# Kernel optimization log

Hardware: AMD Instinct MI355X
Metric: run time of the kernel (lower is better)

Reference implementation:

```python
import jax, jax.numpy as jnp
import numpy as np
import math

HIDDEN = 1024
NUM_HEADS = 16
HEAD_DIM = 64
NUM_PREV = 4
BATCH = 4
SEQ = 1024
ROPE_BASE = 10000.0


def _rope(x):
    """Apply rotary embedding to x [..., seq, head_dim] (rotate-half form)."""
    d = x.shape[-1]
    s = x.shape[-2]
    inv_freq = 1.0 / (ROPE_BASE ** (jnp.arange(0, d, 2, dtype=jnp.float32) / d))
    ang = jnp.arange(s, dtype=jnp.float32)[:, None] * inv_freq[None, :]  # [s, d/2]
    cos, sin = jnp.cos(ang), jnp.sin(ang)
    x1, x2 = jnp.split(x, 2, axis=-1)
    return jnp.concatenate([x1 * cos - x2 * sin, x1 * sin + x2 * cos], axis=-1)


def setup_inputs() -> dict:
    key = jax.random.key(0)
    ks = jax.random.split(key, 8)
    std = 0.02
    d = {
        "hidden_states": jax.random.normal(ks[0], (BATCH, SEQ, HIDDEN), jnp.float32),
        "prev_hidden_states": jax.random.normal(ks[1], (NUM_PREV, BATCH, SEQ, HIDDEN), jnp.float32),
        "wq": jax.random.normal(ks[2], (HIDDEN, NUM_HEADS * HEAD_DIM), jnp.float32) * std,
        "bq": jnp.zeros((NUM_HEADS * HEAD_DIM,), jnp.float32),
        "wk": jax.random.normal(ks[3], (HIDDEN, NUM_HEADS * HEAD_DIM), jnp.float32) * std,
        "bk": jnp.zeros((NUM_HEADS * HEAD_DIM,), jnp.float32),
        "wv": jax.random.normal(ks[4], (HIDDEN, NUM_HEADS * HEAD_DIM), jnp.float32) * std,
        "bv": jnp.zeros((NUM_HEADS * HEAD_DIM,), jnp.float32),
        "wo": jax.random.normal(ks[5], (NUM_HEADS * HEAD_DIM, HIDDEN), jnp.float32) * std,
        "bo": jnp.zeros((HIDDEN,), jnp.float32),
        "wg": jax.random.normal(ks[6], (HIDDEN, NUM_PREV), jnp.float32) * std,
    }
    return d


def reference(hidden_states, prev_hidden_states, wq, bq, wk, bk, wv, bv, wo, bo, wg):
    B, S, H = hidden_states.shape
    P = prev_hidden_states.shape[0]
    nh, hd = NUM_HEADS, HEAD_DIM

    # Q projection + split heads + RoPE: [b, h, s, d]
    q = (hidden_states @ wq + bq).reshape(B, S, nh, hd).transpose(0, 2, 1, 3)
    q = _rope(q)

    # K/V projections for all prev layers at once: [p, b, h, s, d]
    k = (jnp.einsum('pbsh,he->pbse', prev_hidden_states, wk) + bk)
    k = k.reshape(P, B, S, nh, hd).transpose(0, 1, 3, 2, 4)
    k = _rope(k)
    v = (jnp.einsum('pbsh,he->pbse', prev_hidden_states, wv) + bv)
    v = v.reshape(P, B, S, nh, hd).transpose(0, 1, 3, 2, 4)

    # Attention per prev layer
    scale = 1.0 / math.sqrt(hd)
    attn = jnp.einsum('bhqd,pbhkd->pbhqk', q, k) * scale
    attn = jax.nn.softmax(attn, axis=-1)
    out = jnp.einsum('pbhqk,pbhkd->pbhqd', attn, v)  # [p, b, h, s, d]
    out = out.transpose(0, 1, 3, 2, 4).reshape(P, B, S, H)

    # Learned layer gating (faithful to original broadcast: requires B == P)
    pooled = jnp.mean(hidden_states, axis=1)            # [b, hidden]
    layer_w = jax.nn.softmax(pooled @ wg, axis=-1)      # [b, p]
    combined = jnp.sum(out * layer_w[:, :, None, None], axis=0)  # [b, s, hidden]

    return combined @ wo + bo
```

## Files before the change

kernel.cpp:

```cpp
#include <hip/hip_runtime.h>
#include <hip/hip_bf16.h>

#define B_  4
#define S_  1024
#define H_  1024
#define NH  16
#define HD  64
#define P_  4

typedef __attribute__((ext_vector_type(8))) short bf16x8;
typedef __attribute__((ext_vector_type(4))) float f32x4;

__device__ __forceinline__ float b2f(short s) {
  union { unsigned int u; float f; } v;
  v.u = ((unsigned int)(unsigned short)s) << 16;
  return v.f;
}
__device__ __forceinline__ short f2b(float f) {
  __hip_bfloat16 h = __float2bfloat16(f);
  return *reinterpret_cast<short*>(&h);
}
__device__ __forceinline__ float fast_exp2(float x) {
  float r;
  asm volatile("v_exp_f32 %0, %1" : "=v"(r) : "v"(x));
  return r;
}
__device__ __forceinline__ void gload_lds16(const void* g, void* l) {
  __builtin_amdgcn_global_load_lds(
      (const __attribute__((address_space(1))) unsigned int*)((uintptr_t)g),
      (__attribute__((address_space(3))) unsigned int*)((uintptr_t)l),
      16, 0, 0);
}

__global__ void prep_kernel(const float* __restrict__ hidden, const float* __restrict__ prev,
                            const float* __restrict__ wq, const float* __restrict__ wk,
                            const float* __restrict__ wv, const float* __restrict__ wo,
                            short* __restrict__ hbf, short* __restrict__ pbf,
                            short* __restrict__ wqT, short* __restrict__ wkT,
                            short* __restrict__ wvT, short* __restrict__ woT,
                            float* __restrict__ cost, float* __restrict__ sint,
                            float* __restrict__ pooled) {
  __shared__ short tile[32][33];
  int bid = blockIdx.x, tid = threadIdx.x;
  if (bid < 10240) {
    const float* src; short* dst; int idx;
    if (bid < 2048) { src = hidden; dst = hbf; idx = bid * 256 + tid; }
    else            { src = prev;   dst = pbf; idx = (bid - 2048) * 256 + tid; }
    const float4* s4 = (const float4*)(src + (size_t)idx * 8);
    float4 a = s4[0], b = s4[1];
    bf16x8 pk;
    pk[0] = f2b(a.x); pk[1] = f2b(a.y); pk[2] = f2b(a.z); pk[3] = f2b(a.w);
    pk[4] = f2b(b.x); pk[5] = f2b(b.y); pk[6] = f2b(b.z); pk[7] = f2b(b.w);
    *(bf16x8*)(dst + (size_t)idx * 8) = pk;
  } else if (bid < 14336) {
    int tb = bid - 10240;
    int z = tb >> 10, t = tb & 1023;
    const float* src = (z == 0) ? wq : (z == 1) ? wk : (z == 2) ? wv : wo;
    short*       dst = (z == 0) ? wqT : (z == 1) ? wkT : (z == 2) ? wvT : woT;
    int tx = tid & 31, ty = tid >> 5;
    int c0 = (t & 31) * 32, r0 = (t >> 5) * 32;
#pragma unroll
    for (int i = 0; i < 4; ++i)
      tile[ty + 8 * i][tx] = f2b(src[(r0 + ty + 8 * i) * 1024 + c0 + tx]);
    __syncthreads();
#pragma unroll
    for (int i = 0; i < 4; ++i)
      dst[(c0 + ty + 8 * i) * 1024 + r0 + tx] = tile[tx][ty + 8 * i];
  } else if (bid < 14464) {
    int idx = (bid - 14336) * 256 + tid;
    int s = idx >> 5, i = idx & 31;
    float invf = expf(-(float)i * (logf(10000.0f) / 32.0f));
    float a = (float)s * invf;
    cost[idx] = cosf(a);
    sint[idx] = sinf(a);
  } else {
    int idx = (bid - 14464) * 256 + tid;
    int b = idx >> 10, e = idx & 1023;
    const float* hp = hidden + (size_t)b * S_ * H_ + e;
    float s = 0.f;
    for (int t = 0; t < S_; ++t) s += hp[t * H_];
    pooled[idx] = s * (1.0f / 1024.0f);
  }
}

__global__ void gate_kernel(const float* __restrict__ pooled, const float* __restrict__ wg,
                            float* __restrict__ lw) {
  int w = threadIdx.x >> 6, lane = threadIdx.x & 63;
  float a0 = 0.f, a1 = 0.f, a2 = 0.f, a3 = 0.f;
  for (int e = lane; e < 1024; e += 64) {
    float pv = pooled[w * 1024 + e];
    a0 += pv * wg[e * 4 + 0];
    a1 += pv * wg[e * 4 + 1];
    a2 += pv * wg[e * 4 + 2];
    a3 += pv * wg[e * 4 + 3];
  }
#pragma unroll
  for (int off = 32; off > 0; off >>= 1) {
    a0 += __shfl_xor(a0, off, 64);
    a1 += __shfl_xor(a1, off, 64);
    a2 += __shfl_xor(a2, off, 64);
    a3 += __shfl_xor(a3, off, 64);
  }
  if (lane == 0) {
    float mx = fmaxf(fmaxf(a0, a1), fmaxf(a2, a3));
    float e0 = expf(a0 - mx), e1 = expf(a1 - mx), e2 = expf(a2 - mx), e3 = expf(a3 - mx);
    float inv = 1.0f / (e0 + e1 + e2 + e3);
    lw[w * 4 + 0] = e0 * inv;
    lw[w * 4 + 1] = e1 * inv;
    lw[w * 4 + 2] = e2 * inv;
    lw[w * 4 + 3] = e3 * inv;
  }
}

__device__ __forceinline__ void rope_epilogue(const f32x4 (&acc)[4][4], const float* __restrict__ bias,
                                              short* __restrict__ outp,
                                              const float* __restrict__ cost,
                                              const float* __restrict__ sint,
                                              int m0, int wm, int quad, int c, int hh) {
  float b0 = bias[hh * 64 + c];
  float b1 = bias[hh * 64 + 16 + c];
  float b2_ = bias[hh * 64 + 32 + c];
  float b3 = bias[hh * 64 + 48 + c];
#pragma unroll
  for (int mt = 0; mt < 4; ++mt) {
    int gm = m0 + wm * 64 + mt * 16 + quad * 4;
#pragma unroll
    for (int j = 0; j < 4; ++j) {
      int m = gm + j;
      int s = m & 1023;
      int bbx = m >> 10;
      int orow = ((bbx * NH + hh) * S_ + s) * HD;
      float c0f = cost[s * 32 + c], s0f = sint[s * 32 + c];
      float x1 = acc[mt][0][j] + b0, x2 = acc[mt][2][j] + b2_;
      outp[orow + c]      = f2b(x1 * c0f - x2 * s0f);
      outp[orow + 32 + c] = f2b(x1 * s0f + x2 * c0f);
      float c1f = cost[s * 32 + 16 + c], s1f = sint[s * 32 + 16 + c];
      float y1 = acc[mt][1][j] + b1, y2 = acc[mt][3][j] + b3;
      outp[orow + 16 + c] = f2b(y1 * c1f - y2 * s1f);
      outp[orow + 48 + c] = f2b(y1 * s1f + y2 * c1f);
    }
  }
}

__launch_bounds__(256, 2)
__global__ void qkv_gemm(const short* __restrict__ hbf, const short* __restrict__ pbf,
                         const short* __restrict__ BTq, const short* __restrict__ BTk,
                         const short* __restrict__ BTv,
                         const float* __restrict__ bq, const float* __restrict__ bk,
                         const float* __restrict__ bv,
                         short* __restrict__ outq, short* __restrict__ outk,
                         short* __restrict__ outv,
                         const float* __restrict__ cost, const float* __restrict__ sint) {
  __shared__ __align__(16) short As[128 * 64];
  __shared__ __align__(16) short Bs1[128 * 64];
  __shared__ __align__(16) short Bs2[128 * 64];
  int id = blockIdx.x;
  int xcd = id & 7;
  int local = id >> 3;
  int n0i = local & 7;
  int yl = local >> 3;
  int y = yl * 8 + xcd;
  int tid = threadIdx.x;
  int lane = tid & 63, wvv = tid >> 6;
  int quad = lane >> 4, c = lane & 15;
  int wm = wvv & 1, wn = wvv >> 1;
  bool isQ = y < 32;
  int m0 = (isQ ? y : (y - 32)) * 128;
  int n0 = n0i * 128;
  const short* A  = isQ ? hbf : pbf;
  const short* B1 = isQ ? BTq : BTk;
  f32x4 acc1[4][4] = {}, acc2[4][4] = {};
  const short* Ab = A + (size_t)m0 * 1024;
  const short* Bb1 = B1 + (size_t)n0 * 1024;
  const short* Bb2 = BTv + (size_t)n0 * 1024;
  int sr = tid >> 3, sch = tid & 7;

  for (int kb = 0; kb < 16; ++kb) {
    int k0 = kb * 64;
    __syncthreads();
#pragma unroll
    for (int rd = 0; rd < 4; ++rd) {
      int row = sr + rd * 32;
      int col = ((sch ^ (row & 7)) * 8) + k0;
      gload_lds16(Ab + row * 1024 + col,  As  + rd * 2048 + tid * 8);
      gload_lds16(Bb1 + row * 1024 + col, Bs1 + rd * 2048 + tid * 8);
      if (!isQ) gload_lds16(Bb2 + row * 1024 + col, Bs2 + rd * 2048 + tid * 8);
    }
    __syncthreads();
#pragma unroll
    for (int ko = 0; ko < 2; ++ko) {
      bf16x8 af[4], b1f[4];
#pragma unroll
      for (int mt = 0; mt < 4; ++mt) {
        int row = wm * 64 + mt * 16 + c;
        af[mt] = *(const bf16x8*)&As[row * 64 + (((ko * 4 + quad) ^ (row & 7)) * 8)];
      }
#pragma unroll
      for (int nt = 0; nt < 4; ++nt) {
        int row = wn * 64 + nt * 16 + c;
        b1f[nt] = *(const bf16x8*)&Bs1[row * 64 + (((ko * 4 + quad) ^ (row & 7)) * 8)];
      }
#pragma unroll
      for (int mt = 0; mt < 4; ++mt)
#pragma unroll
        for (int nt = 0; nt < 4; ++nt)
          acc1[mt][nt] = __builtin_amdgcn_mfma_f32_16x16x32_bf16(af[mt], b1f[nt], acc1[mt][nt], 0, 0, 0);
      if (!isQ) {
        bf16x8 b2f_[4];
#pragma unroll
        for (int nt = 0; nt < 4; ++nt) {
          int row = wn * 64 + nt * 16 + c;
          b2f_[nt] = *(const bf16x8*)&Bs2[row * 64 + (((ko * 4 + quad) ^ (row & 7)) * 8)];
        }
#pragma unroll
        for (int mt = 0; mt < 4; ++mt)
#pragma unroll
          for (int nt = 0; nt < 4; ++nt)
            acc2[mt][nt] = __builtin_amdgcn_mfma_f32_16x16x32_bf16(af[mt], b2f_[nt], acc2[mt][nt], 0, 0, 0);
      }
    }
  }

  int colb = n0 + wn * 64;
  int hh = colb >> 6;
  if (isQ) {
    rope_epilogue(acc1, bq, outq, cost, sint, m0, wm, quad, c, hh);
  } else {
    rope_epilogue(acc1, bk, outk, cost, sint, m0, wm, quad, c, hh);
    float bb[4];
#pragma unroll
    for (int nt = 0; nt < 4; ++nt) bb[nt] = bv[hh * 64 + nt * 16 + c];
#pragma unroll
    for (int mt = 0; mt < 4; ++mt) {
      int gm = m0 + wm * 64 + mt * 16 + quad * 4;
      int s4 = gm & 1023, pb = gm >> 10;
#pragma unroll
      for (int nt = 0; nt < 4; ++nt) {
        int d = nt * 16 + c;
        ushort4 pk;
        pk.x = (unsigned short)f2b(acc2[mt][nt][0] + bb[nt]);
        pk.y = (unsigned short)f2b(acc2[mt][nt][1] + bb[nt]);
        pk.z = (unsigned short)f2b(acc2[mt][nt][2] + bb[nt]);
        pk.w = (unsigned short)f2b(acc2[mt][nt][3] + bb[nt]);
        *(ushort4*)&outv[((pb * NH + hh) * HD + d) * S_ + s4] = pk;
      }
    }
  }
}

__launch_bounds__(256, 3)
__global__ void attn_kernel(const short* __restrict__ q, const short* __restrict__ k,
                            const short* __restrict__ vt, short* __restrict__ o) {
  int blk = blockIdx.x;
  int x = blk & 7, qt = (blk >> 3) & 7, g = blk >> 6;
  int pbh = g * 8 + x;
  int b = (pbh >> 4) & 3, h = pbh & 15;
  int tid = threadIdx.x;
  int w = tid >> 6, lane = tid & 63, quad = lane >> 4, c = lane & 15;
  int c7 = c & 7;

  __shared__ __align__(16) short Klds[64 * 64];
  __shared__ __align__(16) short Vlds[64 * 64];
  __shared__ __align__(16) short Plds[4][32 * 64];
  __shared__ float lsumf[4][32];

  const short* qbase = q + ((size_t)(b * NH + h) * S_ + qt * 128 + w * 32 + c) * HD;
  bf16x8 aq[2][2];
#pragma unroll
  for (int mi = 0; mi < 2; ++mi) {
    aq[mi][0] = *(const bf16x8*)(qbase + mi * 16 * HD + quad * 8);
    aq[mi][1] = *(const bf16x8*)(qbase + mi * 16 * HD + 32 + quad * 8);
  }

  const short* kb = k + (size_t)pbh * S_ * HD;
  const short* vb = vt + (size_t)pbh * HD * S_;

  f32x4 O[2][4] = {};
  float lsum[2] = {0.f, 0.f};
  const float cs = 0.18033688011f;

  int sr = tid >> 3;
  int lc = (tid & 7) ^ (sr & 7);

  for (int kt = 0; kt < 16; ++kt) {
    __syncthreads();
    const short* ksrc = kb + (kt * 64 + sr) * HD + lc * 8;
    gload_lds16(ksrc,           Klds + tid * 8);
    gload_lds16(ksrc + 32 * HD, Klds + 2048 + tid * 8);
    const short* vsrc = vb + (size_t)sr * S_ + kt * 64 + lc * 8;
    gload_lds16(vsrc,           Vlds + tid * 8);
    gload_lds16(vsrc + 32 * S_, Vlds + 2048 + tid * 8);
    __syncthreads();

    bf16x8 kf[4][2];
#pragma unroll
    for (int t = 0; t < 4; ++t) {
      int row = (t * 16 + c) * 64;
      kf[t][0] = *(const bf16x8*)&Klds[row + (quad ^ c7) * 8];
      kf[t][1] = *(const bf16x8*)&Klds[row + (quad ^ 4 ^ c7) * 8];
    }

#pragma unroll
    for (int mi = 0; mi < 2; ++mi) {
      int rq = mi * 16 + c;
#pragma unroll
      for (int t = 0; t < 4; ++t) {
        f32x4 st = {};
        st = __builtin_amdgcn_mfma_f32_16x16x32_bf16(kf[t][0], aq[mi][0], st, 0, 0, 0);
        st = __builtin_amdgcn_mfma_f32_16x16x32_bf16(kf[t][1], aq[mi][1], st, 0, 0, 0);
        short4 pk4;
        float p0 = fast_exp2(st[0] * cs);
        float p1 = fast_exp2(st[1] * cs);
        float p2 = fast_exp2(st[2] * cs);
        float p3 = fast_exp2(st[3] * cs);
        lsum[mi] += (p0 + p1) + (p2 + p3);
        pk4.x = f2b(p0); pk4.y = f2b(p1); pk4.z = f2b(p2); pk4.w = f2b(p3);
        int chunkL = t * 2 + (quad >> 1);
        *(short4*)&Plds[w][rq * 64 + ((chunkL ^ c7)) * 8 + (quad & 1) * 4] = pk4;
      }
    }

    bf16x8 bv0[4], bv1[4];
#pragma unroll
    for (int nt = 0; nt < 4; ++nt) {
      int row = (nt * 16 + c) * 64;
      bv0[nt] = *(const bf16x8*)&Vlds[row + (quad ^ c7) * 8];
      bv1[nt] = *(const bf16x8*)&Vlds[row + (quad ^ 4 ^ c7) * 8];
    }
#pragma unroll
    for (int mi = 0; mi < 2; ++mi) {
      int prow = (mi * 16 + c) * 64;
      bf16x8 aP0 = *(const bf16x8*)&Plds[w][prow + (quad ^ c7) * 8];
      bf16x8 aP1 = *(const bf16x8*)&Plds[w][prow + (quad ^ 4 ^ c7) * 8];
#pragma unroll
      for (int nt = 0; nt < 4; ++nt) {
        O[mi][nt] = __builtin_amdgcn_mfma_f32_16x16x32_bf16(aP0, bv0[nt], O[mi][nt], 0, 0, 0);
        O[mi][nt] = __builtin_amdgcn_mfma_f32_16x16x32_bf16(aP1, bv1[nt], O[mi][nt], 0, 0, 0);
      }
    }
  }

#pragma unroll
  for (int mi = 0; mi < 2; ++mi) {
    float s = lsum[mi];
    s += __shfl_xor(s, 16, 64);
    s += __shfl_xor(s, 32, 64);
    if (lane < 16) lsumf[w][mi * 16 + c] = s;
  }
#pragma unroll
  for (int mi = 0; mi < 2; ++mi) {
    f32x4 lv = *(const f32x4*)&lsumf[w][mi * 16 + quad * 4];
    short* ob = o + ((size_t)pbh * S_ + qt * 128 + w * 32 + mi * 16 + quad * 4) * HD;
#pragma unroll
    for (int j = 0; j < 4; ++j) {
      float inv = 1.0f / lv[j];
      ob[j * HD + c]      = f2b(O[mi][0][j] * inv);
      ob[j * HD + 16 + c] = f2b(O[mi][1][j] * inv);
      ob[j * HD + 32 + c] = f2b(O[mi][2][j] * inv);
      ob[j * HD + 48 + c] = f2b(O[mi][3][j] * inv);
    }
  }
}

__global__ void combine_kernel(const short* __restrict__ o, const float* __restrict__ lw,
                               short* __restrict__ comb) {
  int idx = blockIdx.x * 256 + threadIdx.x;
  int e8 = idx & 127;
  int s = (idx >> 7) & 1023;
  int b = idx >> 17;
  int h = e8 >> 3, d0 = (e8 & 7) * 8;
  float acc[8] = {};
#pragma unroll
  for (int p = 0; p < 4; ++p) {
    float wgt = lw[p * 4 + b];
    const short* op = o + (((size_t)(p * 4 + b) * NH + h) * S_ + s) * HD + d0;
    bf16x8 v = *(const bf16x8*)op;
#pragma unroll
    for (int i = 0; i < 8; ++i) acc[i] += wgt * b2f(v[i]);
  }
  bf16x8 pk;
#pragma unroll
  for (int i = 0; i < 8; ++i) pk[i] = f2b(acc[i]);
  *(bf16x8*)&comb[((size_t)b * S_ + s) * H_ + e8 * 8] = pk;
}

__launch_bounds__(256, 4)
__global__ void gemm_out(const short* __restrict__ A, const short* __restrict__ BT,
                         const float* __restrict__ bias, float* __restrict__ outf) {
  __shared__ __align__(16) short As[64 * 64];
  __shared__ __align__(16) short Bs[128 * 64];
  int id = blockIdx.x;
  int xcd = id & 7;
  int local = id >> 3;
  int n0i = local & 7;
  int yl = local >> 3;
  int y = yl * 8 + xcd;
  int tid = threadIdx.x;
  int lane = tid & 63, wvv = tid >> 6;
  int quad = lane >> 4, c = lane & 15;
  int wm = wvv & 1, wn = wvv >> 1;
  int m0 = y * 64, n0 = n0i * 128;
  f32x4 acc[2][4] = {};
  const short* Ab = A + (size_t)m0 * 1024;
  const short* Bb = BT + (size_t)n0 * 1024;
  int sr = tid >> 3, sch = tid & 7;

  for (int kb = 0; kb < 16; ++kb) {
    int k0 = kb * 64;
    __syncthreads();
#pragma unroll
    for (int rd = 0; rd < 2; ++rd) {
      int row = sr + rd * 32;
      int col = ((sch ^ (row & 7)) * 8) + k0;
      gload_lds16(Ab + row * 1024 + col, As + rd * 2048 + tid * 8);
    }
#pragma unroll
    for (int rd = 0; rd < 4; ++rd) {
      int row = sr + rd * 32;
      int col = ((sch ^ (row & 7)) * 8) + k0;
      gload_lds16(Bb + row * 1024 + col, Bs + rd * 2048 + tid * 8);
    }
    __syncthreads();
#pragma unroll
    for (int ko = 0; ko < 2; ++ko) {
      bf16x8 af[2], bfr[4];
#pragma unroll
      for (int mt = 0; mt < 2; ++mt) {
        int row = wm * 32 + mt * 16 + c;
        af[mt] = *(const bf16x8*)&As[row * 64 + (((ko * 4 + quad) ^ (row & 7)) * 8)];
      }
#pragma unroll
      for (int nt = 0; nt < 4; ++nt) {
        int row = wn * 64 + nt * 16 + c;
        bfr[nt] = *(const bf16x8*)&Bs[row * 64 + (((ko * 4 + quad) ^ (row & 7)) * 8)];
      }
#pragma unroll
      for (int mt = 0; mt < 2; ++mt)
#pragma unroll
        for (int nt = 0; nt < 4; ++nt)
          acc[mt][nt] = __builtin_amdgcn_mfma_f32_16x16x32_bf16(af[mt], bfr[nt], acc[mt][nt], 0, 0, 0);
    }
  }

  int colb = n0 + wn * 64;
  float bb[4];
#pragma unroll
  for (int nt = 0; nt < 4; ++nt) bb[nt] = bias[colb + nt * 16 + c];
#pragma unroll
  for (int mt = 0; mt < 2; ++mt) {
    int gm = m0 + wm * 32 + mt * 16 + quad * 4;
#pragma unroll
    for (int j = 0; j < 4; ++j) {
      int m = gm + j;
#pragma unroll
      for (int nt = 0; nt < 4; ++nt)
        outf[(size_t)m * 1024 + colb + nt * 16 + c] = acc[mt][nt][j] + bb[nt];
    }
  }
}

extern "C" void kernel_launch(void* const* d_in, const int* in_sizes, int n_in,
                              void* d_out, int out_size, void* d_ws, size_t ws_size,
                              hipStream_t stream) {
  (void)in_sizes; (void)n_in; (void)out_size; (void)ws_size;
  const float* hidden = (const float*)d_in[0];
  const float* prev   = (const float*)d_in[1];
  const float* wq = (const float*)d_in[2];
  const float* bq = (const float*)d_in[3];
  const float* wk = (const float*)d_in[4];
  const float* bk = (const float*)d_in[5];
  const float* wv = (const float*)d_in[6];
  const float* bv = (const float*)d_in[7];
  const float* wo = (const float*)d_in[8];
  const float* bo = (const float*)d_in[9];
  const float* wg = (const float*)d_in[10];
  float* out = (float*)d_out;
  char* ws = (char*)d_ws;

  size_t off = 0;
  short* wqT = (short*)(ws + off); off += (size_t)1024 * 1024 * 2;
  short* wkT = (short*)(ws + off); off += (size_t)1024 * 1024 * 2;
  short* wvT = (short*)(ws + off); off += (size_t)1024 * 1024 * 2;
  short* woT = (short*)(ws + off); off += (size_t)1024 * 1024 * 2;
  short* hbf = (short*)(ws + off); off += (size_t)B_ * S_ * H_ * 2;
  short* pbf = (short*)(ws + off); off += (size_t)P_ * B_ * S_ * H_ * 2;
  short* qbf = (short*)(ws + off); off += (size_t)B_ * S_ * H_ * 2;
  short* kbf = (short*)(ws + off); off += (size_t)P_ * B_ * S_ * H_ * 2;
  short* vtb = (short*)(ws + off); off += (size_t)P_ * B_ * S_ * H_ * 2;
  float* cost = (float*)(ws + off); off += (size_t)S_ * 32 * 4;
  float* sint = (float*)(ws + off); off += (size_t)S_ * 32 * 4;
  float* pooled = (float*)(ws + off); off += (size_t)B_ * H_ * 4;
  float* lw = (float*)(ws + off); off += 64;
  short* obf  = pbf;
  short* comb = qbf;

  prep_kernel<<<14480, 256, 0, stream>>>(hidden, prev, wq, wk, wv, wo,
                                         hbf, pbf, wqT, wkT, wvT, woT,
                                         cost, sint, pooled);
  gate_kernel<<<1, 256, 0, stream>>>(pooled, wg, lw);
  qkv_gemm<<<1280, 256, 0, stream>>>(hbf, pbf, wqT, wkT, wvT,
                                     bq, bk, bv, qbf, kbf, vtb, cost, sint);
  attn_kernel<<<2048, 256, 0, stream>>>(qbf, kbf, vtb, obf);
  combine_kernel<<<2048, 256, 0, stream>>>(obf, lw, comb);
  gemm_out<<<512, 256, 0, stream>>>(comb, woT, bo, out);
}
```

Before: 383.6 us.

## Rewrite attention inner loop with 32x32x16 MFMA and register-resident P

The attention kernel moves from 16x16x32 MFMA tiles to 32x32x16 tiles, computing S^T so the softmax probabilities can be rearranged in registers with v_permlane32_swap instead of going through a per-wave P buffer in LDS. This drops the P LDS round trip and its barrier-free shared traffic, shrinks LDS usage, and raises the launch-bounds occupancy hint from 3 to 4 blocks. The cost is more intricate lane mapping and possible register pressure from the 16-wide accumulators under the tighter occupancy bound.

```diff
diff --git a/kernel.cpp b/kernel.cpp
--- a/kernel.cpp
+++ b/kernel.cpp
@@ -10,6 +10,8 @@
 
 typedef __attribute__((ext_vector_type(8))) short bf16x8;
 typedef __attribute__((ext_vector_type(4))) float f32x4;
+typedef __attribute__((ext_vector_type(16))) float f32x16;
+typedef __attribute__((ext_vector_type(4))) unsigned int u32x4;
 
 __device__ __forceinline__ float b2f(short s) {
   union { unsigned int u; float f; } v;
@@ -248,7 +250,7 @@
   }
 }
 
-__launch_bounds__(256, 3)
+__launch_bounds__(256, 4)
 __global__ void attn_kernel(const short* __restrict__ q, const short* __restrict__ k,
                             const short* __restrict__ vt, short* __restrict__ o) {
   int blk = blockIdx.x;
@@ -256,27 +258,24 @@
   int pbh = g * 8 + x;
   int b = (pbh >> 4) & 3, h = pbh & 15;
   int tid = threadIdx.x;
-  int w = tid >> 6, lane = tid & 63, quad = lane >> 4, c = lane & 15;
-  int c7 = c & 7;
+  int w = tid >> 6, lane = tid & 63;
+  int l31 = lane & 31, hh = lane >> 5;
+  int r7 = l31 & 7;
 
   __shared__ __align__(16) short Klds[64 * 64];
   __shared__ __align__(16) short Vlds[64 * 64];
-  __shared__ __align__(16) short Plds[4][32 * 64];
   __shared__ float lsumf[4][32];
 
-  const short* qbase = q + ((size_t)(b * NH + h) * S_ + qt * 128 + w * 32 + c) * HD;
-  bf16x8 aq[2][2];
-#pragma unroll
-  for (int mi = 0; mi < 2; ++mi) {
-    aq[mi][0] = *(const bf16x8*)(qbase + mi * 16 * HD + quad * 8);
-    aq[mi][1] = *(const bf16x8*)(qbase + mi * 16 * HD + 32 + quad * 8);
-  }
+  const short* qbase = q + ((size_t)(b * NH + h) * S_ + qt * 128 + w * 32 + l31) * HD + hh * 8;
+  bf16x8 aq[4];
+#pragma unroll
+  for (int st4 = 0; st4 < 4; ++st4) aq[st4] = *(const bf16x8*)(qbase + st4 * 16);
 
   const short* kb = k + (size_t)pbh * S_ * HD;
   const short* vb = vt + (size_t)pbh * HD * S_;
 
-  f32x4 O[2][4] = {};
-  float lsum[2] = {0.f, 0.f};
+  f32x16 O0 = {}, O1 = {};
+  float ls0 = 0.f, ls1 = 0.f, ls2 = 0.f, ls3 = 0.f;
   const float cs = 0.18033688011f;
 
   int sr = tid >> 3;
@@ -292,72 +291,63 @@
     gload_lds16(vsrc + 32 * S_, Vlds + 2048 + tid * 8);
     __syncthreads();
 
-    bf16x8 kf[4][2];
-#pragma unroll
-    for (int t = 0; t < 4; ++t) {
-      int row = (t * 16 + c) * 64;
-      kf[t][0] = *(const bf16x8*)&Klds[row + (quad ^ c7) * 8];
-      kf[t][1] = *(const bf16x8*)&Klds[row + (quad ^ 4 ^ c7) * 8];
-    }
-
-#pragma unroll
-    for (int mi = 0; mi < 2; ++mi) {
-      int rq = mi * 16 + c;
-#pragma unroll
-      for (int t = 0; t < 4; ++t) {
-        f32x4 st = {};
-        st = __builtin_amdgcn_mfma_f32_16x16x32_bf16(kf[t][0], aq[mi][0], st, 0, 0, 0);
-        st = __builtin_amdgcn_mfma_f32_16x16x32_bf16(kf[t][1], aq[mi][1], st, 0, 0, 0);
-        short4 pk4;
-        float p0 = fast_exp2(st[0] * cs);
-        float p1 = fast_exp2(st[1] * cs);
-        float p2 = fast_exp2(st[2] * cs);
-        float p3 = fast_exp2(st[3] * cs);
-        lsum[mi] += (p0 + p1) + (p2 + p3);
-        pk4.x = f2b(p0); pk4.y = f2b(p1); pk4.z = f2b(p2); pk4.w = f2b(p3);
-        int chunkL = t * 2 + (quad >> 1);
-        *(short4*)&Plds[w][rq * 64 + ((chunkL ^ c7)) * 8 + (quad & 1) * 4] = pk4;
-      }
-    }
-
-    bf16x8 bv0[4], bv1[4];
-#pragma unroll
-    for (int nt = 0; nt < 4; ++nt) {
-      int row = (nt * 16 + c) * 64;
-      bv0[nt] = *(const bf16x8*)&Vlds[row + (quad ^ c7) * 8];
-      bv1[nt] = *(const bf16x8*)&Vlds[row + (quad ^ 4 ^ c7) * 8];
-    }
-#pragma unroll
-    for (int mi = 0; mi < 2; ++mi) {
-      int prow = (mi * 16 + c) * 64;
-      bf16x8 aP0 = *(const bf16x8*)&Plds[w][prow + (quad ^ c7) * 8];
-      bf16x8 aP1 = *(const bf16x8*)&Plds[w][prow + (quad ^ 4 ^ c7) * 8];
-#pragma unroll
-      for (int nt = 0; nt < 4; ++nt) {
-        O[mi][nt] = __builtin_amdgcn_mfma_f32_16x16x32_bf16(aP0, bv0[nt], O[mi][nt], 0, 0, 0);
-        O[mi][nt] = __builtin_amdgcn_mfma_f32_16x16x32_bf16(aP1, bv1[nt], O[mi][nt], 0, 0, 0);
-      }
-    }
-  }
-
-#pragma unroll
-  for (int mi = 0; mi < 2; ++mi) {
-    float s = lsum[mi];
-    s += __shfl_xor(s, 16, 64);
-    s += __shfl_xor(s, 32, 64);
-    if (lane < 16) lsumf[w][mi * 16 + c] = s;
-  }
-#pragma unroll
-  for (int mi = 0; mi < 2; ++mi) {
-    f32x4 lv = *(const f32x4*)&lsumf[w][mi * 16 + quad * 4];
-    short* ob = o + ((size_t)pbh * S_ + qt * 128 + w * 32 + mi * 16 + quad * 4) * HD;
+    u32x4 pa[4];
+#pragma unroll
+    for (int tau = 0; tau < 2; ++tau) {
+      f32x16 st = {};
+#pragma unroll
+      for (int step = 0; step < 4; ++step) {
+        bf16x8 kf = *(const bf16x8*)&Klds[(tau * 32 + l31) * 64 + (((step * 2 + hh) ^ r7) * 8)];
+        st = __builtin_amdgcn_mfma_f32_32x32x16_bf16(kf, aq[step], st, 0, 0, 0);
+      }
+      unsigned wb[8];
+#pragma unroll
+      for (int m = 0; m < 8; ++m) {
+        float p0 = fast_exp2(st[2 * m] * cs);
+        float p1 = fast_exp2(st[2 * m + 1] * cs);
+        float ps = p0 + p1;
+        if ((m & 3) == 0) ls0 += ps;
+        else if ((m & 3) == 1) ls1 += ps;
+        else if ((m & 3) == 2) ls2 += ps;
+        else ls3 += ps;
+        asm("v_cvt_pk_bf16_f32 %0, %1, %2" : "=v"(wb[m]) : "v"(p0), "v"(p1));
+      }
+#pragma unroll
+      for (int gg = 0; gg < 2; ++gg) {
+        unsigned x0 = wb[4 * gg + 0], y0 = wb[4 * gg + 2];
+        unsigned x1 = wb[4 * gg + 1], y1 = wb[4 * gg + 3];
+        asm volatile("v_permlane32_swap_b32 %0, %1" : "+v"(x0), "+v"(y0));
+        asm volatile("v_permlane32_swap_b32 %0, %1" : "+v"(x1), "+v"(y1));
+        u32x4 paw;
+        paw[0] = x0; paw[1] = x1; paw[2] = y0; paw[3] = y1;
+        pa[2 * tau + gg] = paw;
+      }
+    }
+
+#pragma unroll
+    for (int T = 0; T < 4; ++T) {
+      bf16x8 ap = __builtin_bit_cast(bf16x8, pa[T]);
+      bf16x8 vf0 = *(const bf16x8*)&Vlds[l31 * 64 + (((T * 2 + hh) ^ r7) * 8)];
+      O0 = __builtin_amdgcn_mfma_f32_32x32x16_bf16(ap, vf0, O0, 0, 0, 0);
+      bf16x8 vf1 = *(const bf16x8*)&Vlds[(32 + l31) * 64 + (((T * 2 + hh) ^ r7) * 8)];
+      O1 = __builtin_amdgcn_mfma_f32_32x32x16_bf16(ap, vf1, O1, 0, 0, 0);
+    }
+  }
+
+  float lsum = (ls0 + ls1) + (ls2 + ls3);
+  lsum += __shfl_xor(lsum, 32, 64);
+  if (lane < 32) lsumf[w][l31] = lsum;
+
+  short* ob = o + ((size_t)pbh * S_ + qt * 128 + w * 32) * HD;
+#pragma unroll
+  for (int gg = 0; gg < 4; ++gg) {
+    f32x4 lv = *(const f32x4*)&lsumf[w][4 * hh + 8 * gg];
 #pragma unroll
     for (int j = 0; j < 4; ++j) {
       float inv = 1.0f / lv[j];
-      ob[j * HD + c]      = f2b(O[mi][0][j] * inv);
-      ob[j * HD + 16 + c] = f2b(O[mi][1][j] * inv);
-      ob[j * HD + 32 + c] = f2b(O[mi][2][j] * inv);
-      ob[j * HD + 48 + c] = f2b(O[mi][3][j] * inv);
+      int qrow = 4 * hh + 8 * gg + j;
+      ob[qrow * HD + l31]      = f2b(O0[4 * gg + j] * inv);
+      ob[qrow * HD + 32 + l31] = f2b(O1[4 * gg + j] * inv);
     }
   }
 }
```

Result: no change. 381.9 us (-0.4%).
